# Kernel optimization log

Measured on AMD Instinct MI355X. Metric: run time of the kernel, lower is better.

The kernel has to match this reference:

```python
import jax, jax.numpy as jnp
import numpy as np

N_FEAT = 1024
NEG_INF = -1e30  # stand-in for -inf that is safe in fp32 softmax


def setup_inputs() -> dict:
    key = jax.random.key(0)
    k1, k2 = jax.random.split(key)
    T, C = 4096, N_FEAT
    x = jax.random.normal(k1, (T, C), dtype=jnp.float32)
    W = jax.random.normal(k2, (C, 3 * C), dtype=jnp.float32) * (1.0 / np.sqrt(C))
    b = jnp.zeros((3 * C,), dtype=jnp.float32)
    return {"x": x, "W": W, "b": b, "n_padd": 0}


def reference(x, W, b, n_padd):
    T, C = x.shape
    qkv = x @ W + b                      # [T, 3C]
    q, k, v = jnp.split(qkv, 3, axis=1)  # each [T, C]
    att = (q @ k.T) * (1.0 / jnp.sqrt(jnp.float32(C)))  # [T, T]
    idx = jnp.arange(T)
    # causal mask AND padding mask: only keys >= n_padd for queries >= n_padd
    mask = (idx[None, :] <= idx[:, None]) & (idx[None, :] >= n_padd) & (idx[:, None] >= n_padd)
    att = jnp.where(mask, att, NEG_INF)
    att = jax.nn.softmax(att, axis=-1)
    y = att @ v                          # [T, C]
    return y
```

## Files before the change

### kernel.cpp

```cpp
#include <hip/hip_runtime.h>
#include <hip/hip_bf16.h>
#include <math.h>

#define C_DIM 1024
#define QKS  2048

typedef __attribute__((ext_vector_type(8))) short bf16x8;
typedef __attribute__((ext_vector_type(4))) float f32x4;

__device__ __forceinline__ unsigned short f2bf(float f) {
  __hip_bfloat16 h = __float2bfloat16(f);
  return *(reinterpret_cast<unsigned short*>(&h));
}
__device__ __forceinline__ float bf2f(unsigned short u) {
  return __uint_as_float(((unsigned int)u) << 16);
}
__device__ __forceinline__ f32x4 mfma16(bf16x8 a, bf16x8 b, f32x4 c) {
  return __builtin_amdgcn_mfma_f32_16x16x32_bf16(a, b, c, 0, 0, 0);
}

__device__ __forceinline__ void gload_lds16(const unsigned short* g,
                                            unsigned short* l) {
  __builtin_amdgcn_global_load_lds(
      (const __attribute__((address_space(1))) void*)(g),
      (__attribute__((address_space(3))) void*)(l), 16, 0, 0);
}

__global__ __launch_bounds__(256) void cast_x(
    const float* __restrict__ x, unsigned short* __restrict__ xb) {
  const int i = (blockIdx.x * 256 + threadIdx.x) << 2;
  float4 v = *(const float4*)(x + i);
  ushort4 u;
  u.x = f2bf(v.x); u.y = f2bf(v.y); u.z = f2bf(v.z); u.w = f2bf(v.w);
  *(ushort4*)(xb + i) = u;
}

__global__ __launch_bounds__(256) void transpose_w(
    const float* __restrict__ W, unsigned short* __restrict__ WT) {
  __shared__ float Ls[64][65];
  const int n0 = blockIdx.x * 64;
  const int k0 = blockIdx.y * 64;
  const int c = (threadIdx.x & 15) << 2;
  const int r = threadIdx.x >> 4;
#pragma unroll
  for (int rr = 0; rr < 64; rr += 16) {
    float4 v = *(const float4*)(W + (size_t)(k0 + r + rr) * 3072 + n0 + c);
    Ls[r + rr][c + 0] = v.x; Ls[r + rr][c + 1] = v.y;
    Ls[r + rr][c + 2] = v.z; Ls[r + rr][c + 3] = v.w;
  }
  __syncthreads();
#pragma unroll
  for (int rr = 0; rr < 64; rr += 16) {
    const int X = r + rr;
    ushort4 u;
    u.x = f2bf(Ls[c + 0][X]); u.y = f2bf(Ls[c + 1][X]);
    u.z = f2bf(Ls[c + 2][X]); u.w = f2bf(Ls[c + 3][X]);
    *(ushort4*)(WT + (size_t)(n0 + X) * C_DIM + k0 + c) = u;
  }
}

template <int MODE>
__global__ __launch_bounds__(256) void gemm128(
    const unsigned short* __restrict__ A, const unsigned short* __restrict__ BT,
    void* __restrict__ Cv, const float* __restrict__ bias,
    int lda, int ldb, int ldc, int T) {
  __shared__ __align__(16) unsigned short As[2][128][32];
  __shared__ __align__(16) unsigned short Bs[2][128][32];

  const int tid = threadIdx.x, lane = tid & 63, w = tid >> 6;
  const int qd = lane >> 4, n16 = lane & 15;

  int m0, n0, kbeg, kend;
  bool use_atomic = false;
  if (MODE == 2) {
    if ((int)blockIdx.x > (int)blockIdx.y) return;
    m0 = blockIdx.y * 128; n0 = blockIdx.x * 128; kbeg = 0; kend = C_DIM;
  } else if (MODE == 3) {
    const int nyt = T >> 7;
    const int ex  = nyt > 16 ? nyt - 16 : 0;
    const int by  = (int)blockIdx.y;
    int bi, seg;
    if (by < nyt) { bi = by; seg = 0; } else { bi = by - ex; seg = 1; }
    const int kc = (bi + 1) << 7;
    kbeg = seg ? 2048 : 0;
    kend = seg ? kc : (kc < 2048 ? kc : 2048);
    m0 = bi << 7; n0 = blockIdx.x * 128;
    use_atomic = (kc > 2048);
  } else {
    m0 = blockIdx.y * 128; n0 = blockIdx.x * 128; kbeg = 0; kend = C_DIM;
  }

  f32x4 s[8][2];
#pragma unroll
  for (int mt = 0; mt < 8; ++mt)
#pragma unroll
    for (int j = 0; j < 2; ++j) s[mt][j] = (f32x4){0.f, 0.f, 0.f, 0.f};

  const int srow = lane >> 2;
  const int skc  = (lane & 3) << 3;
  const unsigned short* ag0 = A  + (size_t)(m0 + (w << 5) + srow)      * lda + kbeg + skc;
  const unsigned short* ag1 = A  + (size_t)(m0 + (w << 5) + 16 + srow) * lda + kbeg + skc;
  const unsigned short* bg0 = BT + (size_t)(n0 + (w << 5) + srow)      * ldb + kbeg + skc;
  const unsigned short* bg1 = BT + (size_t)(n0 + (w << 5) + 16 + srow) * ldb + kbeg + skc;

  const int nt = (kend - kbeg) >> 5;

  gload_lds16(ag0, &As[0][(w << 5)][0]);
  gload_lds16(ag1, &As[0][(w << 5) + 16][0]);
  gload_lds16(bg0, &Bs[0][(w << 5)][0]);
  gload_lds16(bg1, &Bs[0][(w << 5) + 16][0]);

  int cur = 0;
  for (int t = 0; t < nt; ++t) {
    __syncthreads();
    if (t + 1 < nt) {
      const int ko = (t + 1) << 5;
      const int nb = cur ^ 1;
      gload_lds16(ag0 + ko, &As[nb][(w << 5)][0]);
      gload_lds16(ag1 + ko, &As[nb][(w << 5) + 16][0]);
      gload_lds16(bg0 + ko, &Bs[nb][(w << 5)][0]);
      gload_lds16(bg1 + ko, &Bs[nb][(w << 5) + 16][0]);
    }
    bf16x8 bf0 = *(const bf16x8*)&Bs[cur][(w << 5) + n16][qd << 3];
    bf16x8 bf1 = *(const bf16x8*)&Bs[cur][(w << 5) + 16 + n16][qd << 3];
#pragma unroll
    for (int mt = 0; mt < 8; ++mt) {
      bf16x8 af = *(const bf16x8*)&As[cur][(mt << 4) + n16][qd << 3];
      s[mt][0] = mfma16(af, bf0, s[mt][0]);
      s[mt][1] = mfma16(af, bf1, s[mt][1]);
    }
    cur ^= 1;
  }

  if (MODE == 3) {
    float* C = (float*)Cv;
#pragma unroll
    for (int mt = 0; mt < 8; ++mt)
#pragma unroll
      for (int j = 0; j < 2; ++j) {
        const int col = n0 + (w << 5) + (j << 4) + n16;
#pragma unroll
        for (int r = 0; r < 4; ++r) {
          const int row = m0 + (mt << 4) + (qd << 2) + r;
          if (use_atomic) atomicAdd(&C[(size_t)row * ldc + col], s[mt][j][r]);
          else            C[(size_t)row * ldc + col] = s[mt][j][r];
        }
      }
  } else {
    unsigned short* C = (unsigned short*)Cv;
#pragma unroll
    for (int mt = 0; mt < 8; ++mt)
#pragma unroll
      for (int j = 0; j < 2; ++j) {
        const int col = n0 + (w << 5) + (j << 4) + n16;
        const float bc = (MODE == 0) ? bias[col] : 0.f;
#pragma unroll
        for (int r = 0; r < 4; ++r) {
          const int row = m0 + (mt << 4) + (qd << 2) + r;
          float v = s[mt][j][r];
          if (MODE == 0) v += bc;
          if (MODE == 1) v += bias[row];
          if (MODE == 2) v *= 0.03125f;
          C[(size_t)row * ldc + col] = f2bf(v);
        }
      }
  }
}

__global__ __launch_bounds__(256) void softmax_rows(
    unsigned short* __restrict__ P, const int* __restrict__ np_p, int T) {
  __shared__ float red[8];
  const int i = blockIdx.x;
  const int np = *np_p;
  const int klen = ((i >> 7) + 1) << 7;
  const int tid = threadIdx.x, lane = tid & 63, w = tid >> 6;
  const int j0 = tid << 4;
  unsigned short* rowp = P + (size_t)i * T;
  const bool act = j0 < klen;

  if (i < np) {
    if (act) {
      uint4 z = {0, 0, 0, 0};
      *(uint4*)(rowp + j0) = z;
      *(uint4*)(rowp + j0 + 8) = z;
    }
    return;
  }

  float v[16];
  float mx = -3.0e38f;
  if (act) {
    uint4 u0 = *(const uint4*)(rowp + j0);
    uint4 u1 = *(const uint4*)(rowp + j0 + 8);
    const unsigned int uu[8] = {u0.x, u0.y, u0.z, u0.w, u1.x, u1.y, u1.z, u1.w};
#pragma unroll
    for (int u = 0; u < 8; ++u) {
      v[2 * u]     = bf2f(uu[u] & 0xffff);
      v[2 * u + 1] = bf2f(uu[u] >> 16);
    }
#pragma unroll
    for (int u = 0; u < 16; ++u) {
      const int j = j0 + u;
      if (j > i || j < np) v[u] = -3.0e38f;
      mx = fmaxf(mx, v[u]);
    }
  }
  mx = fmaxf(mx, __shfl_xor(mx, 32));
  mx = fmaxf(mx, __shfl_xor(mx, 16));
  mx = fmaxf(mx, __shfl_xor(mx, 8));
  mx = fmaxf(mx, __shfl_xor(mx, 4));
  mx = fmaxf(mx, __shfl_xor(mx, 2));
  mx = fmaxf(mx, __shfl_xor(mx, 1));
  if (lane == 0) red[w] = mx;
  __syncthreads();
  const float M = fmaxf(fmaxf(red[0], red[1]), fmaxf(red[2], red[3]));

  float sum = 0.f;
  if (act) {
#pragma unroll
    for (int u = 0; u < 16; ++u) {
      const float p = (v[u] > -1.0e30f) ? __expf(v[u] - M) : 0.f;
      v[u] = p;
      sum += p;
    }
  }
  sum += __shfl_xor(sum, 32);
  sum += __shfl_xor(sum, 16);
  sum += __shfl_xor(sum, 8);
  sum += __shfl_xor(sum, 4);
  sum += __shfl_xor(sum, 2);
  sum += __shfl_xor(sum, 1);
  if (lane == 0) red[4 + w] = sum;
  __syncthreads();
  const float inv = 1.0f / (red[4] + red[5] + red[6] + red[7]);

  if (act) {
    unsigned int o[8];
#pragma unroll
    for (int u = 0; u < 8; ++u) {
      const unsigned int lo = f2bf(v[2 * u] * inv);
      const unsigned int hi = f2bf(v[2 * u + 1] * inv);
      o[u] = lo | (hi << 16);
    }
    uint4 s0 = {o[0], o[1], o[2], o[3]};
    uint4 s1 = {o[4], o[5], o[6], o[7]};
    *(uint4*)(rowp + j0) = s0;
    *(uint4*)(rowp + j0 + 8) = s1;
  }
}

__global__ __launch_bounds__(256) void zero_hi(float* __restrict__ out) {
  const size_t i = ((size_t)blockIdx.x * 256 + threadIdx.x) * 4 +
                   (size_t)2048 * C_DIM;
  float4 z = {0.f, 0.f, 0.f, 0.f};
  *(float4*)(out + i) = z;
}

__global__ __launch_bounds__(256) void padfix(
    const unsigned short* __restrict__ vtb, const int* __restrict__ np_p,
    float* __restrict__ out, int T) {
  const int np = *np_p;
  const int row0 = blockIdx.x * 32;
  if (row0 >= np) return;
  const int pc = min(np - row0, 32);
  const int c4 = threadIdx.x << 2;
  float a[4] = {0.f, 0.f, 0.f, 0.f};
#pragma unroll
  for (int c = 0; c < 4; ++c) {
    const unsigned short* vr = vtb + (size_t)(c4 + c) * T;
    for (int j = 0; j < T; j += 8) {
      uint4 v = *(const uint4*)(vr + j);
      a[c] += bf2f(v.x & 0xffff) + bf2f(v.x >> 16) + bf2f(v.y & 0xffff) + bf2f(v.y >> 16)
            + bf2f(v.z & 0xffff) + bf2f(v.z >> 16) + bf2f(v.w & 0xffff) + bf2f(v.w >> 16);
    }
  }
  const float inv = 1.0f / (float)T;
  float4 rv = {a[0] * inv, a[1] * inv, a[2] * inv, a[3] * inv};
  for (int r = 0; r < pc; ++r)
    *(float4*)(out + (size_t)(row0 + r) * C_DIM + c4) = rv;
}

extern "C" void kernel_launch(void* const* d_in, const int* in_sizes, int n_in,
                              void* d_out, int out_size, void* d_ws, size_t ws_size,
                              hipStream_t stream) {
  const float* x    = (const float*)d_in[0];
  const float* W    = (const float*)d_in[1];
  const float* b    = (const float*)d_in[2];
  const int* n_padd = (const int*)d_in[3];
  float* out = (float*)d_out;

  const int T = in_sizes[0] / C_DIM;
  unsigned short* qkb = (unsigned short*)d_ws;
  unsigned short* vtb = qkb + (size_t)T * QKS;
  unsigned short* xb  = vtb + (size_t)C_DIM * T;
  unsigned short* WT  = xb  + (size_t)T * C_DIM;
  unsigned short* P   = xb;

  cast_x<<<(T * C_DIM) / 1024, 256, 0, stream>>>(x, xb);
  transpose_w<<<dim3(48, 16), 256, 0, stream>>>(W, WT);

  gemm128<0><<<dim3(QKS / 128, T / 128), 256, 0, stream>>>(
      xb, WT, qkb, b, C_DIM, C_DIM, QKS, T);
  gemm128<1><<<dim3(T / 128, C_DIM / 128), 256, 0, stream>>>(
      WT + (size_t)QKS * C_DIM, xb, vtb, b + QKS, C_DIM, C_DIM, T, T);
  gemm128<2><<<dim3(T / 128, T / 128), 256, 0, stream>>>(
      qkb, qkb + C_DIM, P, b, QKS, QKS, T, T);
  softmax_rows<<<T, 256, 0, stream>>>(P, n_padd, T);
  zero_hi<<<((T - 2048) * C_DIM) / 1024, 256, 0, stream>>>(out);
  {
    const int nyt = T / 128;
    const int ex = nyt > 16 ? nyt - 16 : 0;
    gemm128<3><<<dim3(C_DIM / 128, nyt + ex), 256, 0, stream>>>(
        P, vtb, out, b, T, T, C_DIM, T);
  }
  padfix<<<T / 32, 256, 0, stream>>>(vtb, n_padd, out, T);
}
```

Baseline: 248.1 us.

## Shrink GEMM tiles to 128x64 and merge QK and V projections into one launch

Every GEMM now uses a 128x64 tile instead of 128x128, with each wave owning 32 rows across the full 64 columns. This roughly doubles the block count so more CUs are busy and there are fewer partial waves. The QK and V-transpose projection GEMMs are also combined into a single launch with a flattened grid, which removes one kernel launch and lets both sets of tiles share the machine. The cost is lower per-block data reuse: A tiles are reloaded twice as often, so there is more global and LDS traffic per FLOP.

```diff
diff --git a/kernel.cpp b/kernel.cpp
--- a/kernel.cpp
+++ b/kernel.cpp
@@ -4,6 +4,9 @@
 
 #define C_DIM 1024
 #define QKS  2048
+#define BM   128
+#define BN   64
+#define BK   32
 
 typedef __attribute__((ext_vector_type(8))) short bf16x8;
 typedef __attribute__((ext_vector_type(4))) float f32x4;
@@ -60,22 +63,47 @@
 }
 
 template <int MODE>
-__global__ __launch_bounds__(256) void gemm128(
-    const unsigned short* __restrict__ A, const unsigned short* __restrict__ BT,
-    void* __restrict__ Cv, const float* __restrict__ bias,
+__global__ __launch_bounds__(256) void gemm64(
+    const unsigned short* __restrict__ A_, const unsigned short* __restrict__ BT_,
+    void* __restrict__ Cv, const float* __restrict__ bias_,
     int lda, int ldb, int ldc, int T) {
-  __shared__ __align__(16) unsigned short As[2][128][32];
-  __shared__ __align__(16) unsigned short Bs[2][128][32];
+  __shared__ __align__(16) unsigned short As[2][BM][BK];
+  __shared__ __align__(16) unsigned short Bs[2][BN][BK];
 
   const int tid = threadIdx.x, lane = tid & 63, w = tid >> 6;
   const int qd = lane >> 4, n16 = lane & 15;
 
-  int m0, n0, kbeg, kend;
+  const unsigned short* A  = A_;
+  const unsigned short* BT = BT_;
+  const float* bias = bias_;
+  unsigned short* Cb = (unsigned short*)Cv;
+  float* Cf = (float*)Cv;
+  int ldc_ = ldc;
+  int m0, n0, kbeg = 0, kend = C_DIM;
   bool use_atomic = false;
-  if (MODE == 2) {
-    if ((int)blockIdx.x > (int)blockIdx.y) return;
-    m0 = blockIdx.y * 128; n0 = blockIdx.x * 128; kbeg = 0; kend = C_DIM;
-  } else if (MODE == 3) {
+  bool rowbias = false;
+
+  if (MODE == 4) {
+    const int nQKx = QKS / BN;
+    const int nQK  = (T >> 7) * nQKx;
+    int id = (int)blockIdx.x;
+    if (id < nQK) {
+      m0 = (id / nQKx) * BM; n0 = (id % nQKx) * BN;
+    } else {
+      id -= nQK;
+      const int nVx = T / BN;
+      m0 = (id / nVx) * BM; n0 = (id % nVx) * BN;
+      A  = BT_ + (size_t)QKS * C_DIM;
+      BT = A_;
+      Cb = (unsigned short*)Cv + (size_t)T * QKS;
+      bias = bias_ + QKS;
+      rowbias = true;
+      ldc_ = T;
+    }
+  } else if (MODE == 2) {
+    if ((int)(blockIdx.x >> 1) > (int)blockIdx.y) return;
+    m0 = blockIdx.y * BM; n0 = blockIdx.x * BN;
+  } else {
     const int nyt = T >> 7;
     const int ex  = nyt > 16 ? nyt - 16 : 0;
     const int by  = (int)blockIdx.y;
@@ -84,84 +112,79 @@
     const int kc = (bi + 1) << 7;
     kbeg = seg ? 2048 : 0;
     kend = seg ? kc : (kc < 2048 ? kc : 2048);
-    m0 = bi << 7; n0 = blockIdx.x * 128;
+    m0 = bi << 7; n0 = blockIdx.x * BN;
     use_atomic = (kc > 2048);
-  } else {
-    m0 = blockIdx.y * 128; n0 = blockIdx.x * 128; kbeg = 0; kend = C_DIM;
-  }
-
-  f32x4 s[8][2];
-#pragma unroll
-  for (int mt = 0; mt < 8; ++mt)
-#pragma unroll
-    for (int j = 0; j < 2; ++j) s[mt][j] = (f32x4){0.f, 0.f, 0.f, 0.f};
+  }
+
+  f32x4 s[2][4];
+#pragma unroll
+  for (int mt = 0; mt < 2; ++mt)
+#pragma unroll
+    for (int nn = 0; nn < 4; ++nn) s[mt][nn] = (f32x4){0.f, 0.f, 0.f, 0.f};
 
   const int srow = lane >> 2;
   const int skc  = (lane & 3) << 3;
   const unsigned short* ag0 = A  + (size_t)(m0 + (w << 5) + srow)      * lda + kbeg + skc;
   const unsigned short* ag1 = A  + (size_t)(m0 + (w << 5) + 16 + srow) * lda + kbeg + skc;
-  const unsigned short* bg0 = BT + (size_t)(n0 + (w << 5) + srow)      * ldb + kbeg + skc;
-  const unsigned short* bg1 = BT + (size_t)(n0 + (w << 5) + 16 + srow) * ldb + kbeg + skc;
-
-  const int nt = (kend - kbeg) >> 5;
+  const unsigned short* bg0 = BT + (size_t)(n0 + (w << 4) + srow)      * ldb + kbeg + skc;
+
+  const int ntiles = (kend - kbeg) >> 5;
 
   gload_lds16(ag0, &As[0][(w << 5)][0]);
   gload_lds16(ag1, &As[0][(w << 5) + 16][0]);
-  gload_lds16(bg0, &Bs[0][(w << 5)][0]);
-  gload_lds16(bg1, &Bs[0][(w << 5) + 16][0]);
+  gload_lds16(bg0, &Bs[0][(w << 4)][0]);
 
   int cur = 0;
-  for (int t = 0; t < nt; ++t) {
+  for (int t = 0; t < ntiles; ++t) {
     __syncthreads();
-    if (t + 1 < nt) {
+    if (t + 1 < ntiles) {
       const int ko = (t + 1) << 5;
       const int nb = cur ^ 1;
       gload_lds16(ag0 + ko, &As[nb][(w << 5)][0]);
       gload_lds16(ag1 + ko, &As[nb][(w << 5) + 16][0]);
-      gload_lds16(bg0 + ko, &Bs[nb][(w << 5)][0]);
-      gload_lds16(bg1 + ko, &Bs[nb][(w << 5) + 16][0]);
-    }
-    bf16x8 bf0 = *(const bf16x8*)&Bs[cur][(w << 5) + n16][qd << 3];
-    bf16x8 bf1 = *(const bf16x8*)&Bs[cur][(w << 5) + 16 + n16][qd << 3];
-#pragma unroll
-    for (int mt = 0; mt < 8; ++mt) {
-      bf16x8 af = *(const bf16x8*)&As[cur][(mt << 4) + n16][qd << 3];
-      s[mt][0] = mfma16(af, bf0, s[mt][0]);
-      s[mt][1] = mfma16(af, bf1, s[mt][1]);
+      gload_lds16(bg0 + ko, &Bs[nb][(w << 4)][0]);
+    }
+    bf16x8 bf[4];
+#pragma unroll
+    for (int nn = 0; nn < 4; ++nn)
+      bf[nn] = *(const bf16x8*)&Bs[cur][(nn << 4) + n16][qd << 3];
+#pragma unroll
+    for (int mt = 0; mt < 2; ++mt) {
+      bf16x8 af = *(const bf16x8*)&As[cur][(w << 5) + (mt << 4) + n16][qd << 3];
+#pragma unroll
+      for (int nn = 0; nn < 4; ++nn)
+        s[mt][nn] = mfma16(af, bf[nn], s[mt][nn]);
     }
     cur ^= 1;
   }
 
   if (MODE == 3) {
-    float* C = (float*)Cv;
-#pragma unroll
-    for (int mt = 0; mt < 8; ++mt)
-#pragma unroll
-      for (int j = 0; j < 2; ++j) {
-        const int col = n0 + (w << 5) + (j << 4) + n16;
+#pragma unroll
+    for (int mt = 0; mt < 2; ++mt)
+#pragma unroll
+      for (int nn = 0; nn < 4; ++nn) {
+        const int col = n0 + (nn << 4) + n16;
 #pragma unroll
         for (int r = 0; r < 4; ++r) {
-          const int row = m0 + (mt << 4) + (qd << 2) + r;
-          if (use_atomic) atomicAdd(&C[(size_t)row * ldc + col], s[mt][j][r]);
-          else            C[(size_t)row * ldc + col] = s[mt][j][r];
+          const int row = m0 + (w << 5) + (mt << 4) + (qd << 2) + r;
+          if (use_atomic) atomicAdd(&Cf[(size_t)row * ldc_ + col], s[mt][nn][r]);
+          else            Cf[(size_t)row * ldc_ + col] = s[mt][nn][r];
         }
       }
   } else {
-    unsigned short* C = (unsigned short*)Cv;
-#pragma unroll
-    for (int mt = 0; mt < 8; ++mt)
-#pragma unroll
-      for (int j = 0; j < 2; ++j) {
-        const int col = n0 + (w << 5) + (j << 4) + n16;
-        const float bc = (MODE == 0) ? bias[col] : 0.f;
+#pragma unroll
+    for (int mt = 0; mt < 2; ++mt)
+#pragma unroll
+      for (int nn = 0; nn < 4; ++nn) {
+        const int col = n0 + (nn << 4) + n16;
+        const float bc = (MODE == 4 && !rowbias) ? bias[col] : 0.f;
 #pragma unroll
         for (int r = 0; r < 4; ++r) {
-          const int row = m0 + (mt << 4) + (qd << 2) + r;
-          float v = s[mt][j][r];
-          if (MODE == 0) v += bc;
-          if (MODE == 1) v += bias[row];
+          const int row = m0 + (w << 5) + (mt << 4) + (qd << 2) + r;
+          float v = s[mt][nn][r];
+          if (MODE == 4) v += rowbias ? bias[row] : bc;
           if (MODE == 2) v *= 0.03125f;
-          C[(size_t)row * ldc + col] = f2bf(v);
+          Cb[(size_t)row * ldc_ + col] = f2bf(v);
         }
       }
   }
@@ -299,18 +322,20 @@
   cast_x<<<(T * C_DIM) / 1024, 256, 0, stream>>>(x, xb);
   transpose_w<<<dim3(48, 16), 256, 0, stream>>>(W, WT);
 
-  gemm128<0><<<dim3(QKS / 128, T / 128), 256, 0, stream>>>(
-      xb, WT, qkb, b, C_DIM, C_DIM, QKS, T);
-  gemm128<1><<<dim3(T / 128, C_DIM / 128), 256, 0, stream>>>(
-      WT + (size_t)QKS * C_DIM, xb, vtb, b + QKS, C_DIM, C_DIM, T, T);
-  gemm128<2><<<dim3(T / 128, T / 128), 256, 0, stream>>>(
+  {
+    const int nQK = (T / BM) * (QKS / BN);
+    const int nV  = (C_DIM / BM) * (T / BN);
+    gemm64<4><<<nQK + nV, 256, 0, stream>>>(
+        xb, WT, qkb, b, C_DIM, C_DIM, QKS, T);
+  }
+  gemm64<2><<<dim3(T / BN, T / BM), 256, 0, stream>>>(
       qkb, qkb + C_DIM, P, b, QKS, QKS, T, T);
   softmax_rows<<<T, 256, 0, stream>>>(P, n_padd, T);
   zero_hi<<<((T - 2048) * C_DIM) / 1024, 256, 0, stream>>>(out);
   {
-    const int nyt = T / 128;
+    const int nyt = T / BM;
     const int ex = nyt > 16 ? nyt - 16 : 0;
-    gemm128<3><<<dim3(C_DIM / 128, nyt + ex), 256, 0, stream>>>(
+    gemm64<3><<<dim3(C_DIM / BN, nyt + ex), 256, 0, stream>>>(
         P, vtb, out, b, T, T, C_DIM, T);
   }
   padfix<<<T / 32, 256, 0, stream>>>(vtb, n_padd, out, T);
```

After: 241.5 us. -2.7%, faster.

## Fuse all attention stages into one persistent cooperative kernel with fused softmax

Applied to the files above, without the earlier changes.

Replaces the sequence of separate kernels (cast, transpose, QKV GEMMs, QK^T, softmax, PV, pad fix) with a single persistent cooperative kernel that steps through phases separated by grid syncs. The softmax pass is folded into the QK^T epilogue: it writes unnormalized exp values (with no max subtraction) and accumulates row sums atomically, and the PV epilogue divides by those sums. The QK^T phase launches only lower-triangular tiles, and the PV split-K is rebalanced into 1024-wide K chunks. Launch overheads and the full softmax read/write of P go away, at the cost of grid-wide barriers, extra atomics, and a risk of exp overflow because the row max is no longer subtracted.

```diff
diff --git a/kernel.cpp b/kernel.cpp
--- a/kernel.cpp
+++ b/kernel.cpp
@@ -1,9 +1,12 @@
 #include <hip/hip_runtime.h>
+#include <hip/hip_cooperative_groups.h>
 #include <hip/hip_bf16.h>
 #include <math.h>
 
 #define C_DIM 1024
 #define QKS  2048
+
+namespace cg = cooperative_groups;
 
 typedef __attribute__((ext_vector_type(8))) short bf16x8;
 typedef __attribute__((ext_vector_type(4))) float f32x4;
@@ -18,7 +21,6 @@
 __device__ __forceinline__ f32x4 mfma16(bf16x8 a, bf16x8 b, f32x4 c) {
   return __builtin_amdgcn_mfma_f32_16x16x32_bf16(a, b, c, 0, 0, 0);
 }
-
 __device__ __forceinline__ void gload_lds16(const unsigned short* g,
                                             unsigned short* l) {
   __builtin_amdgcn_global_load_lds(
@@ -26,70 +28,22 @@
       (__attribute__((address_space(3))) void*)(l), 16, 0, 0);
 }
 
-__global__ __launch_bounds__(256) void cast_x(
-    const float* __restrict__ x, unsigned short* __restrict__ xb) {
-  const int i = (blockIdx.x * 256 + threadIdx.x) << 2;
-  float4 v = *(const float4*)(x + i);
-  ushort4 u;
-  u.x = f2bf(v.x); u.y = f2bf(v.y); u.z = f2bf(v.z); u.w = f2bf(v.w);
-  *(ushort4*)(xb + i) = u;
-}
-
-__global__ __launch_bounds__(256) void transpose_w(
-    const float* __restrict__ W, unsigned short* __restrict__ WT) {
-  __shared__ float Ls[64][65];
-  const int n0 = blockIdx.x * 64;
-  const int k0 = blockIdx.y * 64;
-  const int c = (threadIdx.x & 15) << 2;
-  const int r = threadIdx.x >> 4;
-#pragma unroll
-  for (int rr = 0; rr < 64; rr += 16) {
-    float4 v = *(const float4*)(W + (size_t)(k0 + r + rr) * 3072 + n0 + c);
-    Ls[r + rr][c + 0] = v.x; Ls[r + rr][c + 1] = v.y;
-    Ls[r + rr][c + 2] = v.z; Ls[r + rr][c + 3] = v.w;
-  }
-  __syncthreads();
-#pragma unroll
-  for (int rr = 0; rr < 64; rr += 16) {
-    const int X = r + rr;
-    ushort4 u;
-    u.x = f2bf(Ls[c + 0][X]); u.y = f2bf(Ls[c + 1][X]);
-    u.z = f2bf(Ls[c + 2][X]); u.w = f2bf(Ls[c + 3][X]);
-    *(ushort4*)(WT + (size_t)(n0 + X) * C_DIM + k0 + c) = u;
-  }
+__device__ __forceinline__ float* rs_addr(unsigned short* P, int r, int T) {
+  return (r < T - 128)
+      ? (float*)(P + (size_t)r * T + (T - 2))
+      : (float*)(P + 256 + ((r - (T - 128)) << 1));
 }
 
 template <int MODE>
-__global__ __launch_bounds__(256) void gemm128(
-    const unsigned short* __restrict__ A, const unsigned short* __restrict__ BT,
-    void* __restrict__ Cv, const float* __restrict__ bias,
-    int lda, int ldb, int ldc, int T) {
-  __shared__ __align__(16) unsigned short As[2][128][32];
-  __shared__ __align__(16) unsigned short Bs[2][128][32];
-
+__device__ void gemm_tile(
+    const unsigned short* A, const unsigned short* BT, void* Cv,
+    const float* bias, int lda, int ldb, int ldc, int T, int np,
+    int m0, int n0, int kbeg, int kend, bool use_atomic, bool rowbias,
+    unsigned short (*As)[128][32], unsigned short (*Bs)[128][32],
+    unsigned short* Prs) {
   const int tid = threadIdx.x, lane = tid & 63, w = tid >> 6;
   const int qd = lane >> 4, n16 = lane & 15;
 
-  int m0, n0, kbeg, kend;
-  bool use_atomic = false;
-  if (MODE == 2) {
-    if ((int)blockIdx.x > (int)blockIdx.y) return;
-    m0 = blockIdx.y * 128; n0 = blockIdx.x * 128; kbeg = 0; kend = C_DIM;
-  } else if (MODE == 3) {
-    const int nyt = T >> 7;
-    const int ex  = nyt > 16 ? nyt - 16 : 0;
-    const int by  = (int)blockIdx.y;
-    int bi, seg;
-    if (by < nyt) { bi = by; seg = 0; } else { bi = by - ex; seg = 1; }
-    const int kc = (bi + 1) << 7;
-    kbeg = seg ? 2048 : 0;
-    kend = seg ? kc : (kc < 2048 ? kc : 2048);
-    m0 = bi << 7; n0 = blockIdx.x * 128;
-    use_atomic = (kc > 2048);
-  } else {
-    m0 = blockIdx.y * 128; n0 = blockIdx.x * 128; kbeg = 0; kend = C_DIM;
-  }
-
   f32x4 s[8][2];
 #pragma unroll
   for (int mt = 0; mt < 8; ++mt)
@@ -98,10 +52,10 @@
 
   const int srow = lane >> 2;
   const int skc  = (lane & 3) << 3;
-  const unsigned short* ag0 = A  + (size_t)(m0 + (w << 5) + srow)      * lda + kbeg + skc;
-  const unsigned short* ag1 = A  + (size_t)(m0 + (w << 5) + 16 + srow) * lda + kbeg + skc;
-  const unsigned short* bg0 = BT + (size_t)(n0 + (w << 5) + srow)      * ldb + kbeg + skc;
-  const unsigned short* bg1 = BT + (size_t)(n0 + (w << 5) + 16 + srow) * ldb + kbeg + skc;
+  const unsigned short* ag0 = A  + (size_t)(m0 + (w << 5) + srow) * lda + kbeg + skc;
+  const unsigned short* ag1 = ag0 + (size_t)16 * lda;
+  const unsigned short* bg0 = BT + (size_t)(n0 + (w << 5) + srow) * ldb + kbeg + skc;
+  const unsigned short* bg1 = bg0 + (size_t)16 * ldb;
 
   const int nt = (kend - kbeg) >> 5;
 
@@ -115,11 +69,11 @@
     __syncthreads();
     if (t + 1 < nt) {
       const int ko = (t + 1) << 5;
-      const int nb = cur ^ 1;
-      gload_lds16(ag0 + ko, &As[nb][(w << 5)][0]);
-      gload_lds16(ag1 + ko, &As[nb][(w << 5) + 16][0]);
-      gload_lds16(bg0 + ko, &Bs[nb][(w << 5)][0]);
-      gload_lds16(bg1 + ko, &Bs[nb][(w << 5) + 16][0]);
+      const int nbuf = cur ^ 1;
+      gload_lds16(ag0 + ko, &As[nbuf][(w << 5)][0]);
+      gload_lds16(ag1 + ko, &As[nbuf][(w << 5) + 16][0]);
+      gload_lds16(bg0 + ko, &Bs[nbuf][(w << 5)][0]);
+      gload_lds16(bg1 + ko, &Bs[nbuf][(w << 5) + 16][0]);
     }
     bf16x8 bf0 = *(const bf16x8*)&Bs[cur][(w << 5) + n16][qd << 3];
     bf16x8 bf1 = *(const bf16x8*)&Bs[cur][(w << 5) + 16 + n16][qd << 3];
@@ -132,152 +86,202 @@
     cur ^= 1;
   }
 
-  if (MODE == 3) {
-    float* C = (float*)Cv;
+  if (MODE == 4) {
+    unsigned short* Cb = (unsigned short*)Cv;
 #pragma unroll
     for (int mt = 0; mt < 8; ++mt)
 #pragma unroll
       for (int j = 0; j < 2; ++j) {
         const int col = n0 + (w << 5) + (j << 4) + n16;
+        const float bc = rowbias ? 0.f : bias[col];
 #pragma unroll
         for (int r = 0; r < 4; ++r) {
           const int row = m0 + (mt << 4) + (qd << 2) + r;
-          if (use_atomic) atomicAdd(&C[(size_t)row * ldc + col], s[mt][j][r]);
-          else            C[(size_t)row * ldc + col] = s[mt][j][r];
-        }
-      }
-  } else {
-    unsigned short* C = (unsigned short*)Cv;
-#pragma unroll
-    for (int mt = 0; mt < 8; ++mt)
+          const float v = s[mt][j][r] + (rowbias ? bias[row] : bc);
+          Cb[(size_t)row * ldc + col] = f2bf(v);
+        }
+      }
+  } else if (MODE == 2) {
+    unsigned short* Cb = (unsigned short*)Cv;
+#pragma unroll
+    for (int mt = 0; mt < 8; ++mt) {
+      const int rowb = m0 + (mt << 4) + (qd << 2);
+      float rsum[4] = {0.f, 0.f, 0.f, 0.f};
 #pragma unroll
       for (int j = 0; j < 2; ++j) {
         const int col = n0 + (w << 5) + (j << 4) + n16;
-        const float bc = (MODE == 0) ? bias[col] : 0.f;
 #pragma unroll
         for (int r = 0; r < 4; ++r) {
-          const int row = m0 + (mt << 4) + (qd << 2) + r;
-          float v = s[mt][j][r];
-          if (MODE == 0) v += bc;
-          if (MODE == 1) v += bias[row];
-          if (MODE == 2) v *= 0.03125f;
-          C[(size_t)row * ldc + col] = f2bf(v);
-        }
-      }
-  }
-}
-
-__global__ __launch_bounds__(256) void softmax_rows(
-    unsigned short* __restrict__ P, const int* __restrict__ np_p, int T) {
-  __shared__ float red[8];
-  const int i = blockIdx.x;
-  const int np = *np_p;
-  const int klen = ((i >> 7) + 1) << 7;
-  const int tid = threadIdx.x, lane = tid & 63, w = tid >> 6;
-  const int j0 = tid << 4;
-  unsigned short* rowp = P + (size_t)i * T;
-  const bool act = j0 < klen;
-
-  if (i < np) {
-    if (act) {
-      uint4 z = {0, 0, 0, 0};
-      *(uint4*)(rowp + j0) = z;
-      *(uint4*)(rowp + j0 + 8) = z;
-    }
-    return;
-  }
-
-  float v[16];
-  float mx = -3.0e38f;
-  if (act) {
-    uint4 u0 = *(const uint4*)(rowp + j0);
-    uint4 u1 = *(const uint4*)(rowp + j0 + 8);
-    const unsigned int uu[8] = {u0.x, u0.y, u0.z, u0.w, u1.x, u1.y, u1.z, u1.w};
-#pragma unroll
-    for (int u = 0; u < 8; ++u) {
-      v[2 * u]     = bf2f(uu[u] & 0xffff);
-      v[2 * u + 1] = bf2f(uu[u] >> 16);
-    }
-#pragma unroll
-    for (int u = 0; u < 16; ++u) {
-      const int j = j0 + u;
-      if (j > i || j < np) v[u] = -3.0e38f;
-      mx = fmaxf(mx, v[u]);
-    }
-  }
-  mx = fmaxf(mx, __shfl_xor(mx, 32));
-  mx = fmaxf(mx, __shfl_xor(mx, 16));
-  mx = fmaxf(mx, __shfl_xor(mx, 8));
-  mx = fmaxf(mx, __shfl_xor(mx, 4));
-  mx = fmaxf(mx, __shfl_xor(mx, 2));
-  mx = fmaxf(mx, __shfl_xor(mx, 1));
-  if (lane == 0) red[w] = mx;
-  __syncthreads();
-  const float M = fmaxf(fmaxf(red[0], red[1]), fmaxf(red[2], red[3]));
-
-  float sum = 0.f;
-  if (act) {
-#pragma unroll
-    for (int u = 0; u < 16; ++u) {
-      const float p = (v[u] > -1.0e30f) ? __expf(v[u] - M) : 0.f;
-      v[u] = p;
-      sum += p;
-    }
-  }
-  sum += __shfl_xor(sum, 32);
-  sum += __shfl_xor(sum, 16);
-  sum += __shfl_xor(sum, 8);
-  sum += __shfl_xor(sum, 4);
-  sum += __shfl_xor(sum, 2);
-  sum += __shfl_xor(sum, 1);
-  if (lane == 0) red[4 + w] = sum;
-  __syncthreads();
-  const float inv = 1.0f / (red[4] + red[5] + red[6] + red[7]);
-
-  if (act) {
-    unsigned int o[8];
-#pragma unroll
-    for (int u = 0; u < 8; ++u) {
-      const unsigned int lo = f2bf(v[2 * u] * inv);
-      const unsigned int hi = f2bf(v[2 * u + 1] * inv);
-      o[u] = lo | (hi << 16);
-    }
-    uint4 s0 = {o[0], o[1], o[2], o[3]};
-    uint4 s1 = {o[4], o[5], o[6], o[7]};
-    *(uint4*)(rowp + j0) = s0;
-    *(uint4*)(rowp + j0 + 8) = s1;
-  }
-}
-
-__global__ __launch_bounds__(256) void zero_hi(float* __restrict__ out) {
-  const size_t i = ((size_t)blockIdx.x * 256 + threadIdx.x) * 4 +
-                   (size_t)2048 * C_DIM;
-  float4 z = {0.f, 0.f, 0.f, 0.f};
-  *(float4*)(out + i) = z;
-}
-
-__global__ __launch_bounds__(256) void padfix(
-    const unsigned short* __restrict__ vtb, const int* __restrict__ np_p,
-    float* __restrict__ out, int T) {
-  const int np = *np_p;
-  const int row0 = blockIdx.x * 32;
-  if (row0 >= np) return;
-  const int pc = min(np - row0, 32);
-  const int c4 = threadIdx.x << 2;
-  float a[4] = {0.f, 0.f, 0.f, 0.f};
-#pragma unroll
-  for (int c = 0; c < 4; ++c) {
-    const unsigned short* vr = vtb + (size_t)(c4 + c) * T;
-    for (int j = 0; j < T; j += 8) {
-      uint4 v = *(const uint4*)(vr + j);
-      a[c] += bf2f(v.x & 0xffff) + bf2f(v.x >> 16) + bf2f(v.y & 0xffff) + bf2f(v.y >> 16)
-            + bf2f(v.z & 0xffff) + bf2f(v.z >> 16) + bf2f(v.w & 0xffff) + bf2f(v.w >> 16);
-    }
-  }
-  const float inv = 1.0f / (float)T;
-  float4 rv = {a[0] * inv, a[1] * inv, a[2] * inv, a[3] * inv};
-  for (int r = 0; r < pc; ++r)
-    *(float4*)(out + (size_t)(row0 + r) * C_DIM + c4) = rv;
+          const int row = rowb + r;
+          float p = 0.f;
+          if (col <= row && col >= np && row >= np)
+            p = __expf(s[mt][j][r] * 0.03125f);
+          Cb[(size_t)row * ldc + col] = f2bf(p);
+          rsum[r] += p;
+        }
+      }
+#pragma unroll
+      for (int r = 0; r < 4; ++r) {
+        rsum[r] += __shfl_xor(rsum[r], 1);
+        rsum[r] += __shfl_xor(rsum[r], 2);
+        rsum[r] += __shfl_xor(rsum[r], 4);
+        rsum[r] += __shfl_xor(rsum[r], 8);
+      }
+      if (n16 == 0) {
+#pragma unroll
+        for (int r = 0; r < 4; ++r)
+          atomicAdd(rs_addr(Prs, rowb + r, T), rsum[r]);
+      }
+    }
+  } else {
+    float* Cf = (float*)Cv;
+#pragma unroll
+    for (int mt = 0; mt < 8; ++mt) {
+      const int rowb = m0 + (mt << 4) + (qd << 2);
+      float inv[4];
+#pragma unroll
+      for (int r = 0; r < 4; ++r)
+        inv[r] = 1.0f / fmaxf(*rs_addr(Prs, rowb + r, T), 1e-37f);
+#pragma unroll
+      for (int j = 0; j < 2; ++j) {
+        const int col = n0 + (w << 5) + (j << 4) + n16;
+#pragma unroll
+        for (int r = 0; r < 4; ++r) {
+          const float v = s[mt][j][r] * inv[r];
+          if (use_atomic) atomicAdd(&Cf[(size_t)(rowb + r) * ldc + col], v);
+          else            Cf[(size_t)(rowb + r) * ldc + col] = v;
+        }
+      }
+    }
+  }
+}
+
+__global__ __launch_bounds__(256, 4) void attn_all(
+    const float* x, const float* W, const float* b, const int* np_p,
+    float* out, unsigned short* ws, int T, int plo, int phi) {
+  __shared__ __align__(16) unsigned char smem[32768];
+  unsigned short (*As)[128][32] = (unsigned short(*)[128][32])smem;
+  unsigned short (*Bs)[128][32] = (unsigned short(*)[128][32])(smem + 16384);
+
+  unsigned short* qkb = ws;
+  unsigned short* vtb = qkb + (size_t)T * QKS;
+  unsigned short* xb  = vtb + (size_t)C_DIM * T;
+  unsigned short* WT  = xb  + (size_t)T * C_DIM;
+  unsigned short* P   = xb;
+
+  const int nb = (int)gridDim.x, bid = (int)blockIdx.x, tid = threadIdx.x;
+  const int g = bid * 256 + tid, nthr = nb * 256;
+  const int tq = T >> 7;
+
+  for (int ph = plo; ph <= phi; ++ph) {
+    if (ph == 0) {
+      const int n4 = (T * C_DIM) >> 2;
+      for (int i = g; i < n4; i += nthr) {
+        float4 v = *(const float4*)(x + ((size_t)i << 2));
+        ushort4 u;
+        u.x = f2bf(v.x); u.y = f2bf(v.y); u.z = f2bf(v.z); u.w = f2bf(v.w);
+        *(ushort4*)(xb + ((size_t)i << 2)) = u;
+      }
+      const int nz4 = ((T - C_DIM) * C_DIM) >> 2;
+      const float4 z = {0.f, 0.f, 0.f, 0.f};
+      for (int i = g; i < nz4; i += nthr)
+        *(float4*)(out + (size_t)C_DIM * C_DIM + ((size_t)i << 2)) = z;
+      float (*Ls)[65] = (float(*)[65])smem;
+      const int c = (tid & 15) << 2, r = tid >> 4;
+      for (int tI = bid; tI < 768; tI += nb) {
+        const int n0 = (tI % 48) << 6, k0 = (tI / 48) << 6;
+        __syncthreads();
+#pragma unroll
+        for (int rr = 0; rr < 64; rr += 16) {
+          float4 v = *(const float4*)(W + (size_t)(k0 + r + rr) * 3072 + n0 + c);
+          Ls[r + rr][c + 0] = v.x; Ls[r + rr][c + 1] = v.y;
+          Ls[r + rr][c + 2] = v.z; Ls[r + rr][c + 3] = v.w;
+        }
+        __syncthreads();
+#pragma unroll
+        for (int rr = 0; rr < 64; rr += 16) {
+          const int X = r + rr;
+          ushort4 u;
+          u.x = f2bf(Ls[c + 0][X]); u.y = f2bf(Ls[c + 1][X]);
+          u.z = f2bf(Ls[c + 2][X]); u.w = f2bf(Ls[c + 3][X]);
+          *(ushort4*)(WT + (size_t)(n0 + X) * C_DIM + k0 + c) = u;
+        }
+      }
+    } else if (ph == 1) {
+      const int nQKx = QKS >> 7;
+      const int nQK  = tq * nQKx;
+      const int nTot = nQK + (C_DIM >> 7) * tq;
+      for (int id = bid; id < nTot; id += nb) {
+        if (id < nQK) {
+          gemm_tile<4>(xb, WT, qkb, b, C_DIM, C_DIM, QKS, T, 0,
+                       (id / nQKx) << 7, (id % nQKx) << 7, 0, C_DIM,
+                       false, false, As, Bs, (unsigned short*)0);
+        } else {
+          const int iv = id - nQK;
+          gemm_tile<4>(WT + (size_t)QKS * C_DIM, xb, vtb, b + QKS,
+                       C_DIM, C_DIM, T, T, 0,
+                       (iv / tq) << 7, (iv % tq) << 7, 0, C_DIM,
+                       false, true, As, Bs, (unsigned short*)0);
+        }
+      }
+    } else if (ph == 2) {
+      for (int r2 = g; r2 < T; r2 += nthr) *rs_addr(P, r2, T) = 0.f;
+    } else if (ph == 3) {
+      const int np = *np_p;
+      const int ntri = tq * (tq + 1) / 2;
+      for (int id = bid; id < ntri; id += nb) {
+        int by = (int)((sqrtf((float)(8 * id + 1)) - 1.0f) * 0.5f);
+        while ((by + 1) * (by + 2) / 2 <= id) ++by;
+        while (by * (by + 1) / 2 > id) --by;
+        const int bx = id - by * (by + 1) / 2;
+        gemm_tile<2>(qkb, qkb + C_DIM, P, b, QKS, QKS, T, T, np,
+                     by << 7, bx << 7, 0, C_DIM, false, false, As, Bs, P);
+      }
+    } else if (ph == 4) {
+      int tot = 0;
+      for (int bi = 0; bi < tq; ++bi) tot += (bi >> 3) + 1;
+      tot <<= 3;
+      for (int id = bid; id < tot; id += nb) {
+        int rem = id, bi = 0;
+        while (rem >= (((bi >> 3) + 1) << 3)) { rem -= ((bi >> 3) + 1) << 3; ++bi; }
+        const int sK = rem >> 3, nx = rem & 7;
+        const int kfull = (bi + 1) << 7;
+        const int kbeg = sK << 10;
+        const int kend = (kbeg + 1024 < kfull) ? kbeg + 1024 : kfull;
+        gemm_tile<3>(P, vtb, out, b, T, T, C_DIM, T, 0,
+                     bi << 7, nx << 7, kbeg, kend, kfull > 1024, false,
+                     As, Bs, P);
+      }
+    } else {
+      const int np = *np_p;
+      for (int id = bid; id < (T >> 5); id += nb) {
+        const int row0 = id << 5;
+        if (row0 >= np) continue;
+        const int pc = min(np - row0, 32);
+        const int c4 = tid << 2;
+        float a[4] = {0.f, 0.f, 0.f, 0.f};
+#pragma unroll
+        for (int cch = 0; cch < 4; ++cch) {
+          const unsigned short* vr = vtb + (size_t)(c4 + cch) * T;
+          for (int j = 0; j < T; j += 8) {
+            uint4 v = *(const uint4*)(vr + j);
+            a[cch] += bf2f(v.x & 0xffff) + bf2f(v.x >> 16)
+                    + bf2f(v.y & 0xffff) + bf2f(v.y >> 16)
+                    + bf2f(v.z & 0xffff) + bf2f(v.z >> 16)
+                    + bf2f(v.w & 0xffff) + bf2f(v.w >> 16);
+          }
+        }
+        const float inv = 1.0f / (float)T;
+        float4 rv = {a[0] * inv, a[1] * inv, a[2] * inv, a[3] * inv};
+        for (int r2 = 0; r2 < pc; ++r2)
+          *(float4*)(out + (size_t)(row0 + r2) * C_DIM + c4) = rv;
+      }
+    }
+    if (ph < phi) {
+      __threadfence();
+      cg::this_grid().sync();
+    }
+  }
 }
 
 extern "C" void kernel_launch(void* const* d_in, const int* in_sizes, int n_in,
@@ -288,30 +292,32 @@
   const float* b    = (const float*)d_in[2];
   const int* n_padd = (const int*)d_in[3];
   float* out = (float*)d_out;
+  unsigned short* ws = (unsigned short*)d_ws;
 
   const int T = in_sizes[0] / C_DIM;
-  unsigned short* qkb = (unsigned short*)d_ws;
-  unsigned short* vtb = qkb + (size_t)T * QKS;
-  unsigned short* xb  = vtb + (size_t)C_DIM * T;
-  unsigned short* WT  = xb  + (size_t)T * C_DIM;
-  unsigned short* P   = xb;
-
-  cast_x<<<(T * C_DIM) / 1024, 256, 0, stream>>>(x, xb);
-  transpose_w<<<dim3(48, 16), 256, 0, stream>>>(W, WT);
-
-  gemm128<0><<<dim3(QKS / 128, T / 128), 256, 0, stream>>>(
-      xb, WT, qkb, b, C_DIM, C_DIM, QKS, T);
-  gemm128<1><<<dim3(T / 128, C_DIM / 128), 256, 0, stream>>>(
-      WT + (size_t)QKS * C_DIM, xb, vtb, b + QKS, C_DIM, C_DIM, T, T);
-  gemm128<2><<<dim3(T / 128, T / 128), 256, 0, stream>>>(
-      qkb, qkb + C_DIM, P, b, QKS, QKS, T, T);
-  softmax_rows<<<T, 256, 0, stream>>>(P, n_padd, T);
-  zero_hi<<<((T - 2048) * C_DIM) / 1024, 256, 0, stream>>>(out);
-  {
-    const int nyt = T / 128;
-    const int ex = nyt > 16 ? nyt - 16 : 0;
-    gemm128<3><<<dim3(C_DIM / 128, nyt + ex), 256, 0, stream>>>(
-        P, vtb, out, b, T, T, C_DIM, T);
-  }
-  padfix<<<T / 32, 256, 0, stream>>>(vtb, n_padd, out, T);
-}
+
+  static int s_grid = -1;
+  if (s_grid < 0) {
+    int mab = 0;
+    hipOccupancyMaxActiveBlocksPerMultiprocessor(&mab, attn_all, 256, 0);
+    hipDeviceProp_t prop;
+    int dev = 0;
+    hipGetDevice(&dev);
+    hipGetDeviceProperties(&prop, dev);
+    int gr = mab * prop.multiProcessorCount;
+    if (gr < 256) gr = 256;
+    if (gr > 1024) gr = 1024;
+    s_grid = gr;
+  }
+
+  int Tl = T, plo = 0, phi = 5;
+  void* args[] = {(void*)&x, (void*)&W, (void*)&b, (void*)&n_padd,
+                  (void*)&out, (void*)&ws, (void*)&Tl, (void*)&plo, (void*)&phi};
+  hipError_t e = hipLaunchCooperativeKernel((void*)attn_all, dim3(s_grid),
+                                            dim3(256), args, 0, stream);
+  if (e != hipSuccess) {
+    for (int ph = 0; ph <= 5; ++ph)
+      attn_all<<<dim3(s_grid), dim3(256), 0, stream>>>(
+          x, W, b, n_padd, out, ws, T, ph, ph);
+  }
+}
```

Result: slower. 800.5 us (+222.7%).
